# Performance work log

Measured on AMD Instinct MI355X. Metric: run time of the kernel, lower is better.

## Reference

```python
import jax, jax.numpy as jnp
import numpy as np

NUM_SAMPLES = 100  # hard-coded in the original forward


def _bilinear(img, x, y):
    """Bilinear sample img (H,W) at pixel coords x,y (any shape); border padding.
    Matches F.grid_sample(align_corners=True, padding_mode='border') since the
    original normalizes by (W-1)/(H-1) which maps back to the same pixel coords."""
    H, W = img.shape
    x0 = jnp.floor(x); y0 = jnp.floor(y)
    wx = x - x0; wy = y - y0
    x0i = jnp.clip(x0, 0, W - 1).astype(jnp.int32)
    x1i = jnp.clip(x0 + 1, 0, W - 1).astype(jnp.int32)
    y0i = jnp.clip(y0, 0, H - 1).astype(jnp.int32)
    y1i = jnp.clip(y0 + 1, 0, H - 1).astype(jnp.int32)
    return (img[y0i, x0i] * (1 - wx) * (1 - wy)
            + img[y0i, x1i] * wx * (1 - wy)
            + img[y1i, x0i] * (1 - wx) * wy
            + img[y1i, x1i] * wx * wy)


def setup_inputs() -> dict:
    key = jax.random.key(0)
    k1, k2, k3 = jax.random.split(key, 3)
    H = W = 2048
    N = 100000
    distance_image = jax.random.uniform(k1, (H, W), dtype=jnp.float32)
    points = jax.random.uniform(k2, (N, 2), dtype=jnp.float32) * (H - 1)
    normals = jax.random.normal(k3, (N, 2), dtype=jnp.float32)
    return {"distance_image": distance_image, "points": points, "normals": normals}


def reference(distance_image, points, normals):
    H, W = distance_image.shape
    N = points.shape[0]
    # original clamps both coords to [0, max(H-1, W-1)]
    pts = jnp.clip(points, 0.0, float(max(H - 1, W - 1)))  # (N,2)

    # direction perpendicular to normal, normalized
    d = jnp.stack([-normals[:, 1], normals[:, 0]], axis=-1)
    d = d / jnp.linalg.norm(d, axis=-1, keepdims=True)  # (N,2)
    dx, dy = d[:, 0], d[:, 1]
    px, py = pts[:, 0], pts[:, 1]

    maxf = jnp.finfo(d.dtype).max
    sdx = jnp.where(dx != 0, dx, 1.0)
    sdy = jnp.where(dy != 0, dy, 1.0)
    t_left = jnp.where(dx != 0, (0.0 - px) / sdx, -maxf)
    t_right = jnp.where(dx != 0, (W - 1.0 - px) / sdx, maxf)
    t_top = jnp.where(dy != 0, (0.0 - py) / sdy, -maxf)
    t_bottom = jnp.where(dy != 0, (H - 1.0 - py) / sdy, maxf)
    t_min = jnp.maximum(t_left, t_top)
    t_max = jnp.minimum(t_right, t_bottom)

    p1 = pts + t_min[:, None] * d  # (N,2)
    p2 = pts + t_max[:, None] * d  # (N,2)

    ts = jnp.linspace(0.0, 1.0, NUM_SAMPLES, dtype=pts.dtype)  # (S,)
    line = p1[:, None, :] + ts[None, :, None] * (p2 - p1)[:, None, :]  # (N,S,2)
    lx = jnp.clip(line[..., 0], 0.0, W - 1.0)
    ly = jnp.clip(line[..., 1], 0.0, H - 1.0)
    line = jnp.stack([lx, ly], axis=-1)  # clamped sampled points (N,S,2)

    vals = _bilinear(distance_image, lx, ly)  # (N,S)
    ref_val = _bilinear(distance_image, px, py)  # (N,)

    # local minima: strict minimum vs both neighbors, indices shifted by +1
    center = vals[:, 1:-1]
    minima = (center < vals[:, :-2]) & (center < vals[:, 2:])  # (N,S-2)

    # distance from each candidate (interior sample points) to the reference point
    dist = jnp.linalg.norm(line[:, 1:-1, :] - pts[:, None, :], axis=-1)  # (N,S-2)
    dist = jnp.where(minima, dist, jnp.inf)
    nearest = jnp.argmin(dist, axis=1)  # (N,)
    nearest_val = vals[jnp.arange(N), nearest + 1]  # (N,)

    # per-point mse of two scalars, then mean over points
    return jnp.mean((nearest_val - ref_val) ** 2)
```

## Files before the change

### kernel.cpp

```cpp
#include <hip/hip_runtime.h>
#include <float.h>
#include <math.h>

#define NSAMP 100
#define IMG_W 2048
#define IMG_H 2048

typedef _Float16 h2_t __attribute__((ext_vector_type(2), aligned(4)));
typedef _Float16 h4_t __attribute__((ext_vector_type(4), aligned(8)));
typedef _Float16 h8_t __attribute__((ext_vector_type(8), aligned(16)));

__global__ __launch_bounds__(256) void convert_kernel(const float* __restrict__ in,
                                                      h2_t* __restrict__ V,
                                                      double* __restrict__ accum,
                                                      unsigned int* __restrict__ done) {
    int idx = blockIdx.x * blockDim.x + threadIdx.x;
    if (idx == 0) { *accum = 0.0; *done = 0u; }
    int y  = idx >> 9;
    int x4 = (idx & 511) << 2;
    int y1 = min(y + 1, IMG_H - 1);
    float4 a = *(const float4*)(in + (size_t)y  * IMG_W + x4);
    float4 b = *(const float4*)(in + (size_t)y1 * IMG_W + x4);
    h8_t o;
    o[0] = (_Float16)a.x; o[1] = (_Float16)b.x;
    o[2] = (_Float16)a.y; o[3] = (_Float16)b.y;
    o[4] = (_Float16)a.z; o[5] = (_Float16)b.z;
    o[6] = (_Float16)a.w; o[7] = (_Float16)b.w;
    *(h8_t*)(V + (size_t)y * IMG_W + x4) = o;
}

__device__ __forceinline__ float bilinV(const h2_t* __restrict__ V, float x, float y) {
    float x0f = floorf(x), y0f = floorf(y);
    float wx = x - x0f, wy = y - y0f;
    int x0 = (int)x0f;
    int y0 = (int)y0f;
    int xa = min(x0, IMG_W - 2);
    bool edge = (x0 == IMG_W - 1);
    h4_t q = *(const h4_t*)(V + (size_t)y0 * IMG_W + xa);
    float v00 = edge ? (float)q[2] : (float)q[0];
    float v10 = edge ? (float)q[3] : (float)q[1];
    float v01 = (float)q[2];
    float v11 = (float)q[3];
    return v00 * (1.f - wx) * (1.f - wy) + v01 * wx * (1.f - wy)
         + v10 * (1.f - wx) * wy       + v11 * wx * wy;
}

__device__ __forceinline__ float tparam(int s) {
    return (s == NSAMP - 1) ? 1.0f : (float)((double)s * (1.0 / 99.0));
}

__global__ __launch_bounds__(256) void contour_loss_kernel(
        const h2_t* __restrict__ V,
        const float* __restrict__ points,
        const float* __restrict__ normals,
        double* __restrict__ accum,
        unsigned int* __restrict__ done,
        float* __restrict__ out,
        int N, int nblocks) {
    int i = blockIdx.x * blockDim.x + threadIdx.x;
    float sq = 0.f;
    if (i < N) {
        float px = fminf(fmaxf(points[2 * i],     0.f), 2047.f);
        float py = fminf(fmaxf(points[2 * i + 1], 0.f), 2047.f);
        float nx = normals[2 * i];
        float ny = normals[2 * i + 1];
        float ddx = -ny, ddy = nx;
        float nrm = sqrtf(ddx * ddx + ddy * ddy);
        float dx = ddx / nrm, dy = ddy / nrm;

        const float maxf = FLT_MAX;
        float sdx = (dx != 0.f) ? dx : 1.f;
        float sdy = (dy != 0.f) ? dy : 1.f;
        float t_left   = (dx != 0.f) ? (0.f    - px) / sdx : -maxf;
        float t_right  = (dx != 0.f) ? (2047.f - px) / sdx :  maxf;
        float t_top    = (dy != 0.f) ? (0.f    - py) / sdy : -maxf;
        float t_bottom = (dy != 0.f) ? (2047.f - py) / sdy :  maxf;
        float t_min = fmaxf(t_left, t_top);
        float t_max = fminf(t_right, t_bottom);

        float p1x = px + t_min * dx, p1y = py + t_min * dy;
        float p2x = px + t_max * dx, p2y = py + t_max * dy;
        float vx = p2x - p1x, vy = p2y - p1y;

        float ref_val = bilinV(V, px, py);

        float lx = fminf(fmaxf(p1x, 0.f), 2047.f);
        float ly = fminf(fmaxf(p1y, 0.f), 2047.f);
        float v_im1 = bilinV(V, lx, ly);
        float t1 = tparam(1);
        lx = fminf(fmaxf(p1x + t1 * vx, 0.f), 2047.f);
        ly = fminf(fmaxf(p1y + t1 * vy, 0.f), 2047.f);
        float v_i = bilinV(V, lx, ly);
        float cx = lx, cy = ly;

        float best_val = v_i;
        float best_d2  = INFINITY;

        #pragma unroll 8
        for (int s = 2; s < NSAMP; ++s) {
            float ts = tparam(s);
            float nlx = fminf(fmaxf(p1x + ts * vx, 0.f), 2047.f);
            float nly = fminf(fmaxf(p1y + ts * vy, 0.f), 2047.f);
            float v_ip1 = bilinV(V, nlx, nly);
            if (v_i < v_im1 && v_i < v_ip1) {
                float ex = cx - px, ey = cy - py;
                float d2 = ex * ex + ey * ey;
                if (d2 < best_d2) { best_d2 = d2; best_val = v_i; }
            }
            v_im1 = v_i; v_i = v_ip1; cx = nlx; cy = nly;
        }
        float diff = best_val - ref_val;
        sq = diff * diff;
    }

    for (int off = 32; off > 0; off >>= 1)
        sq += __shfl_down(sq, off);
    __shared__ float wsum[4];
    int lane = threadIdx.x & 63;
    int wid  = threadIdx.x >> 6;
    if (lane == 0) wsum[wid] = sq;
    __syncthreads();
    if (threadIdx.x == 0) {
        float bs = wsum[0] + wsum[1] + wsum[2] + wsum[3];
        atomicAdd(accum, (double)bs);
        __threadfence();
        unsigned int prev = atomicAdd(done, 1u);
        if (prev == (unsigned int)(nblocks - 1)) {
            double total = atomicAdd(accum, 0.0);
            out[0] = (float)(total / (double)N);
        }
    }
}

extern "C" void kernel_launch(void* const* d_in, const int* in_sizes, int n_in,
                              void* d_out, int out_size, void* d_ws, size_t ws_size,
                              hipStream_t stream) {
    const float* img     = (const float*)d_in[0];
    const float* points  = (const float*)d_in[1];
    const float* normals = (const float*)d_in[2];
    int N = in_sizes[1] / 2;
    float* out = (float*)d_out;

    char* ws = (char*)d_ws;
    h2_t* V = (h2_t*)ws;
    size_t off = (size_t)IMG_W * IMG_H * sizeof(h2_t);
    double* accum      = (double*)(ws + off);  off += 8;
    unsigned int* done = (unsigned int*)(ws + off);

    int conv_blocks = (IMG_W * IMG_H / 4) / 256;
    convert_kernel<<<conv_blocks, 256, 0, stream>>>(img, V, accum, done);

    int grid = (N + 255) / 256;
    contour_loss_kernel<<<grid, 256, 0, stream>>>(V, points, normals,
                                                  accum, done, out, N, grid);
}
```

Before: 128.9 us.

## Split each line's samples across four lanes with shuffle-based argmin merge

Each point is now handled by four consecutive threads, each scanning a 25-sample chunk of the line, followed by an xor-shuffle reduction that picks the nearest minimum and breaks ties by index. The goal is more parallelism: with only 100k points, the old one-thread-per-point launch gave few waves and a long serial latency chain of gathers. In exchange, each point's setup math and reference sample are recomputed four times, and each chunk boundary adds extra gathers.

```diff
diff --git a/kernel.cpp b/kernel.cpp
--- a/kernel.cpp
+++ b/kernel.cpp
@@ -5,6 +5,8 @@
 #define NSAMP 100
 #define IMG_W 2048
 #define IMG_H 2048
+#define LPP 4
+#define CPL 25
 
 typedef _Float16 h2_t __attribute__((ext_vector_type(2), aligned(4)));
 typedef _Float16 h4_t __attribute__((ext_vector_type(4), aligned(8)));
@@ -57,14 +59,16 @@
         unsigned int* __restrict__ done,
         float* __restrict__ out,
         int N, int nblocks) {
-    int i = blockIdx.x * blockDim.x + threadIdx.x;
+    int tid = blockIdx.x * blockDim.x + threadIdx.x;
+    int p = tid >> 2;
+    int k = tid & 3;
     float sq = 0.f;
-    if (i < N) {
-        float px = fminf(fmaxf(points[2 * i],     0.f), 2047.f);
-        float py = fminf(fmaxf(points[2 * i + 1], 0.f), 2047.f);
-        float nx = normals[2 * i];
-        float ny = normals[2 * i + 1];
-        float ddx = -ny, ddy = nx;
+    if (p < N) {
+        float2 pt = *(const float2*)(points  + 2 * (size_t)p);
+        float2 nm = *(const float2*)(normals + 2 * (size_t)p);
+        float px = fminf(fmaxf(pt.x, 0.f), 2047.f);
+        float py = fminf(fmaxf(pt.y, 0.f), 2047.f);
+        float ddx = -nm.y, ddy = nm.x;
         float nrm = sqrtf(ddx * ddx + ddy * ddy);
         float dx = ddx / nrm, dy = ddy / nrm;
 
@@ -84,33 +88,54 @@
 
         float ref_val = bilinV(V, px, py);
 
-        float lx = fminf(fmaxf(p1x, 0.f), 2047.f);
-        float ly = fminf(fmaxf(p1y, 0.f), 2047.f);
-        float v_im1 = bilinV(V, lx, ly);
-        float t1 = tparam(1);
-        lx = fminf(fmaxf(p1x + t1 * vx, 0.f), 2047.f);
-        ly = fminf(fmaxf(p1y + t1 * vy, 0.f), 2047.f);
-        float v_i = bilinV(V, lx, ly);
-        float cx = lx, cy = ly;
+        int cbase = k * CPL;
+        int sm1 = cbase - 1; if (sm1 < 0) sm1 = 0;
+        float ts = tparam(sm1);
+        float blx = fminf(fmaxf(p1x + ts * vx, 0.f), 2047.f);
+        float bly = fminf(fmaxf(p1y + ts * vy, 0.f), 2047.f);
+        float v_im1 = bilinV(V, blx, bly);
+        ts = tparam(cbase);
+        float cx = fminf(fmaxf(p1x + ts * vx, 0.f), 2047.f);
+        float cy = fminf(fmaxf(p1y + ts * vy, 0.f), 2047.f);
+        float v_i = bilinV(V, cx, cy);
 
-        float best_val = v_i;
+        float best_val = 0.f;
         float best_d2  = INFINITY;
+        int   best_idx = 0x7FFFFFFF;
+        float val_s1   = 0.f;
 
-        #pragma unroll 8
-        for (int s = 2; s < NSAMP; ++s) {
-            float ts = tparam(s);
-            float nlx = fminf(fmaxf(p1x + ts * vx, 0.f), 2047.f);
-            float nly = fminf(fmaxf(p1y + ts * vy, 0.f), 2047.f);
+        #pragma unroll 5
+        for (int j = 0; j < CPL; ++j) {
+            int c = cbase + j;
+            int sn = c + 1; if (sn > NSAMP - 1) sn = NSAMP - 1;
+            float tsn = tparam(sn);
+            float nlx = fminf(fmaxf(p1x + tsn * vx, 0.f), 2047.f);
+            float nly = fminf(fmaxf(p1y + tsn * vy, 0.f), 2047.f);
             float v_ip1 = bilinV(V, nlx, nly);
-            if (v_i < v_im1 && v_i < v_ip1) {
+            if (c == 1) val_s1 = v_i;
+            if (c >= 1 && c <= NSAMP - 2 && v_i < v_im1 && v_i < v_ip1) {
                 float ex = cx - px, ey = cy - py;
                 float d2 = ex * ex + ey * ey;
-                if (d2 < best_d2) { best_d2 = d2; best_val = v_i; }
+                if (d2 < best_d2) { best_d2 = d2; best_val = v_i; best_idx = c; }
             }
             v_im1 = v_i; v_i = v_ip1; cx = nlx; cy = nly;
         }
-        float diff = best_val - ref_val;
-        sq = diff * diff;
+
+        #pragma unroll
+        for (int m = 1; m < LPP; m <<= 1) {
+            float od2  = __shfl_xor(best_d2, m);
+            float oval = __shfl_xor(best_val, m);
+            int   oidx = __shfl_xor(best_idx, m);
+            if (od2 < best_d2 || (od2 == best_d2 && oidx < best_idx)) {
+                best_d2 = od2; best_val = oval; best_idx = oidx;
+            }
+        }
+
+        if (k == 0) {
+            if (best_idx == 0x7FFFFFFF) best_val = val_s1;
+            float diff = best_val - ref_val;
+            sq = diff * diff;
+        }
     }
 
     for (int off = 32; off > 0; off >>= 1)
@@ -150,7 +175,7 @@
     int conv_blocks = (IMG_W * IMG_H / 4) / 256;
     convert_kernel<<<conv_blocks, 256, 0, stream>>>(img, V, accum, done);
 
-    int grid = (N + 255) / 256;
+    int grid = (4 * N + 255) / 256;
     contour_loss_kernel<<<grid, 256, 0, stream>>>(V, points, normals,
                                                   accum, done, out, N, grid);
 }
```

New measurement: 180.4 us. 40.0% more time.

## Store image as plain fp16 and fetch two rows per bilinear sample

Applied to the files above, without the earlier changes.

Replaces the interleaved row-pair fp16 table (4 bytes per pixel) with a plain fp16 copy of the image (2 bytes per pixel). This halves the convert kernel's write traffic and the gather kernel's working set. In exchange, each bilinear sample now issues two 4-byte-aligned 8-byte loads, one per row, instead of one, with extra select logic for odd x. Point and normal loads are also vectorized to float2.

```diff
diff --git a/kernel.cpp b/kernel.cpp
--- a/kernel.cpp
+++ b/kernel.cpp
@@ -6,41 +6,39 @@
 #define IMG_W 2048
 #define IMG_H 2048
 
-typedef _Float16 h2_t __attribute__((ext_vector_type(2), aligned(4)));
-typedef _Float16 h4_t __attribute__((ext_vector_type(4), aligned(8)));
-typedef _Float16 h8_t __attribute__((ext_vector_type(8), aligned(16)));
+typedef _Float16 h4w_t __attribute__((ext_vector_type(4), aligned(8)));
+typedef _Float16 h4r_t __attribute__((ext_vector_type(4), aligned(4)));
 
 __global__ __launch_bounds__(256) void convert_kernel(const float* __restrict__ in,
-                                                      h2_t* __restrict__ V,
+                                                      _Float16* __restrict__ T,
                                                       double* __restrict__ accum,
                                                       unsigned int* __restrict__ done) {
     int idx = blockIdx.x * blockDim.x + threadIdx.x;
     if (idx == 0) { *accum = 0.0; *done = 0u; }
     int y  = idx >> 9;
     int x4 = (idx & 511) << 2;
-    int y1 = min(y + 1, IMG_H - 1);
-    float4 a = *(const float4*)(in + (size_t)y  * IMG_W + x4);
-    float4 b = *(const float4*)(in + (size_t)y1 * IMG_W + x4);
-    h8_t o;
-    o[0] = (_Float16)a.x; o[1] = (_Float16)b.x;
-    o[2] = (_Float16)a.y; o[3] = (_Float16)b.y;
-    o[4] = (_Float16)a.z; o[5] = (_Float16)b.z;
-    o[6] = (_Float16)a.w; o[7] = (_Float16)b.w;
-    *(h8_t*)(V + (size_t)y * IMG_W + x4) = o;
+    float4 a = *(const float4*)(in + (size_t)y * IMG_W + x4);
+    h4w_t o;
+    o[0] = (_Float16)a.x; o[1] = (_Float16)a.y;
+    o[2] = (_Float16)a.z; o[3] = (_Float16)a.w;
+    *(h4w_t*)(T + (size_t)y * IMG_W + x4) = o;
 }
 
-__device__ __forceinline__ float bilinV(const h2_t* __restrict__ V, float x, float y) {
+__device__ __forceinline__ float bilinT(const _Float16* __restrict__ T, float x, float y) {
     float x0f = floorf(x), y0f = floorf(y);
     float wx = x - x0f, wy = y - y0f;
     int x0 = (int)x0f;
     int y0 = (int)y0f;
-    int xa = min(x0, IMG_W - 2);
+    int y1 = min(y0 + 1, IMG_H - 1);
+    int xa = x0 & ~1;
+    bool odd  = (x0 & 1) != 0;
     bool edge = (x0 == IMG_W - 1);
-    h4_t q = *(const h4_t*)(V + (size_t)y0 * IMG_W + xa);
-    float v00 = edge ? (float)q[2] : (float)q[0];
-    float v10 = edge ? (float)q[3] : (float)q[1];
-    float v01 = (float)q[2];
-    float v11 = (float)q[3];
+    h4r_t r0 = *(const h4r_t*)(T + (y0 << 11) + xa);
+    h4r_t r1 = *(const h4r_t*)(T + (y1 << 11) + xa);
+    float v00 = odd ? (float)r0[1] : (float)r0[0];
+    float v10 = odd ? (float)r1[1] : (float)r1[0];
+    float v01 = edge ? (float)r0[1] : (odd ? (float)r0[2] : (float)r0[1]);
+    float v11 = edge ? (float)r1[1] : (odd ? (float)r1[2] : (float)r1[1]);
     return v00 * (1.f - wx) * (1.f - wy) + v01 * wx * (1.f - wy)
          + v10 * (1.f - wx) * wy       + v11 * wx * wy;
 }
@@ -50,7 +48,7 @@
 }
 
 __global__ __launch_bounds__(256) void contour_loss_kernel(
-        const h2_t* __restrict__ V,
+        const _Float16* __restrict__ T,
         const float* __restrict__ points,
         const float* __restrict__ normals,
         double* __restrict__ accum,
@@ -60,11 +58,11 @@
     int i = blockIdx.x * blockDim.x + threadIdx.x;
     float sq = 0.f;
     if (i < N) {
-        float px = fminf(fmaxf(points[2 * i],     0.f), 2047.f);
-        float py = fminf(fmaxf(points[2 * i + 1], 0.f), 2047.f);
-        float nx = normals[2 * i];
-        float ny = normals[2 * i + 1];
-        float ddx = -ny, ddy = nx;
+        float2 pt = *(const float2*)(points  + 2 * (size_t)i);
+        float2 nm = *(const float2*)(normals + 2 * (size_t)i);
+        float px = fminf(fmaxf(pt.x, 0.f), 2047.f);
+        float py = fminf(fmaxf(pt.y, 0.f), 2047.f);
+        float ddx = -nm.y, ddy = nm.x;
         float nrm = sqrtf(ddx * ddx + ddy * ddy);
         float dx = ddx / nrm, dy = ddy / nrm;
 
@@ -82,15 +80,15 @@
         float p2x = px + t_max * dx, p2y = py + t_max * dy;
         float vx = p2x - p1x, vy = p2y - p1y;
 
-        float ref_val = bilinV(V, px, py);
+        float ref_val = bilinT(T, px, py);
 
         float lx = fminf(fmaxf(p1x, 0.f), 2047.f);
         float ly = fminf(fmaxf(p1y, 0.f), 2047.f);
-        float v_im1 = bilinV(V, lx, ly);
+        float v_im1 = bilinT(T, lx, ly);
         float t1 = tparam(1);
         lx = fminf(fmaxf(p1x + t1 * vx, 0.f), 2047.f);
         ly = fminf(fmaxf(p1y + t1 * vy, 0.f), 2047.f);
-        float v_i = bilinV(V, lx, ly);
+        float v_i = bilinT(T, lx, ly);
         float cx = lx, cy = ly;
 
         float best_val = v_i;
@@ -101,7 +99,7 @@
             float ts = tparam(s);
             float nlx = fminf(fmaxf(p1x + ts * vx, 0.f), 2047.f);
             float nly = fminf(fmaxf(p1y + ts * vy, 0.f), 2047.f);
-            float v_ip1 = bilinV(V, nlx, nly);
+            float v_ip1 = bilinT(T, nlx, nly);
             if (v_i < v_im1 && v_i < v_ip1) {
                 float ex = cx - px, ey = cy - py;
                 float d2 = ex * ex + ey * ey;
@@ -142,15 +140,15 @@
     float* out = (float*)d_out;
 
     char* ws = (char*)d_ws;
-    h2_t* V = (h2_t*)ws;
-    size_t off = (size_t)IMG_W * IMG_H * sizeof(h2_t);
+    _Float16* T = (_Float16*)ws;
+    size_t off = (size_t)16 * 1024 * 1024;
     double* accum      = (double*)(ws + off);  off += 8;
     unsigned int* done = (unsigned int*)(ws + off);
 
     int conv_blocks = (IMG_W * IMG_H / 4) / 256;
-    convert_kernel<<<conv_blocks, 256, 0, stream>>>(img, V, accum, done);
+    convert_kernel<<<conv_blocks, 256, 0, stream>>>(img, T, accum, done);
 
     int grid = (N + 255) / 256;
-    contour_loss_kernel<<<grid, 256, 0, stream>>>(V, points, normals,
+    contour_loss_kernel<<<grid, 256, 0, stream>>>(T, points, normals,
                                                   accum, done, out, N, grid);
 }
```

Measured after the change: 155.6 us. 1.21x slower.

## Use 64-thread blocks with striped atomic accumulators and vectorized point loads

Applied to the files above, without the earlier changes.

Shrinks the loss kernel to one wavefront per block, which removes the shared-memory block reduction and barrier and spreads the work over more blocks. The per-block partial sums go to eight padded double accumulators instead of one, to reduce contention on a single atomic address, and the last block adds the slots together. It also loads points and normals as float2, uses a 32-bit shift for the row offset, and raises the unroll factor. The cost is four times as many blocks, and therefore four times as many atomics on the done counter.

```diff
diff --git a/kernel.cpp b/kernel.cpp
--- a/kernel.cpp
+++ b/kernel.cpp
@@ -5,6 +5,8 @@
 #define NSAMP 100
 #define IMG_W 2048
 #define IMG_H 2048
+#define NSLOT 8
+#define SLOT_STRIDE 16
 
 typedef _Float16 h2_t __attribute__((ext_vector_type(2), aligned(4)));
 typedef _Float16 h4_t __attribute__((ext_vector_type(4), aligned(8)));
@@ -15,7 +17,11 @@
                                                       double* __restrict__ accum,
                                                       unsigned int* __restrict__ done) {
     int idx = blockIdx.x * blockDim.x + threadIdx.x;
-    if (idx == 0) { *accum = 0.0; *done = 0u; }
+    if (idx == 0) {
+        #pragma unroll
+        for (int s = 0; s < NSLOT; ++s) accum[s * SLOT_STRIDE] = 0.0;
+        *done = 0u;
+    }
     int y  = idx >> 9;
     int x4 = (idx & 511) << 2;
     int y1 = min(y + 1, IMG_H - 1);
@@ -36,7 +42,7 @@
     int y0 = (int)y0f;
     int xa = min(x0, IMG_W - 2);
     bool edge = (x0 == IMG_W - 1);
-    h4_t q = *(const h4_t*)(V + (size_t)y0 * IMG_W + xa);
+    h4_t q = *(const h4_t*)(V + (y0 << 11) + xa);
     float v00 = edge ? (float)q[2] : (float)q[0];
     float v10 = edge ? (float)q[3] : (float)q[1];
     float v01 = (float)q[2];
@@ -49,7 +55,7 @@
     return (s == NSAMP - 1) ? 1.0f : (float)((double)s * (1.0 / 99.0));
 }
 
-__global__ __launch_bounds__(256) void contour_loss_kernel(
+__global__ __launch_bounds__(64) void contour_loss_kernel(
         const h2_t* __restrict__ V,
         const float* __restrict__ points,
         const float* __restrict__ normals,
@@ -60,11 +66,11 @@
     int i = blockIdx.x * blockDim.x + threadIdx.x;
     float sq = 0.f;
     if (i < N) {
-        float px = fminf(fmaxf(points[2 * i],     0.f), 2047.f);
-        float py = fminf(fmaxf(points[2 * i + 1], 0.f), 2047.f);
-        float nx = normals[2 * i];
-        float ny = normals[2 * i + 1];
-        float ddx = -ny, ddy = nx;
+        float2 pt = *(const float2*)(points  + 2 * (size_t)i);
+        float2 nm = *(const float2*)(normals + 2 * (size_t)i);
+        float px = fminf(fmaxf(pt.x, 0.f), 2047.f);
+        float py = fminf(fmaxf(pt.y, 0.f), 2047.f);
+        float ddx = -nm.y, ddy = nm.x;
         float nrm = sqrtf(ddx * ddx + ddy * ddy);
         float dx = ddx / nrm, dy = ddy / nrm;
 
@@ -96,7 +102,7 @@
         float best_val = v_i;
         float best_d2  = INFINITY;
 
-        #pragma unroll 8
+        #pragma unroll 14
         for (int s = 2; s < NSAMP; ++s) {
             float ts = tparam(s);
             float nlx = fminf(fmaxf(p1x + ts * vx, 0.f), 2047.f);
@@ -115,18 +121,15 @@
 
     for (int off = 32; off > 0; off >>= 1)
         sq += __shfl_down(sq, off);
-    __shared__ float wsum[4];
-    int lane = threadIdx.x & 63;
-    int wid  = threadIdx.x >> 6;
-    if (lane == 0) wsum[wid] = sq;
-    __syncthreads();
     if (threadIdx.x == 0) {
-        float bs = wsum[0] + wsum[1] + wsum[2] + wsum[3];
-        atomicAdd(accum, (double)bs);
+        atomicAdd(&accum[(blockIdx.x & (NSLOT - 1)) * SLOT_STRIDE], (double)sq);
         __threadfence();
         unsigned int prev = atomicAdd(done, 1u);
         if (prev == (unsigned int)(nblocks - 1)) {
-            double total = atomicAdd(accum, 0.0);
+            double total = 0.0;
+            #pragma unroll
+            for (int s = 0; s < NSLOT; ++s)
+                total += atomicAdd(&accum[s * SLOT_STRIDE], 0.0);
             out[0] = (float)(total / (double)N);
         }
     }
@@ -144,13 +147,13 @@
     char* ws = (char*)d_ws;
     h2_t* V = (h2_t*)ws;
     size_t off = (size_t)IMG_W * IMG_H * sizeof(h2_t);
-    double* accum      = (double*)(ws + off);  off += 8;
+    double* accum      = (double*)(ws + off);  off += NSLOT * SLOT_STRIDE * sizeof(double);
     unsigned int* done = (unsigned int*)(ws + off);
 
     int conv_blocks = (IMG_W * IMG_H / 4) / 256;
     convert_kernel<<<conv_blocks, 256, 0, stream>>>(img, V, accum, done);
 
-    int grid = (N + 255) / 256;
-    contour_loss_kernel<<<grid, 256, 0, stream>>>(V, points, normals,
-                                                  accum, done, out, N, grid);
+    int grid = (N + 63) / 64;
+    contour_loss_kernel<<<grid, 64, 0, stream>>>(V, points, normals,
+                                                 accum, done, out, N, grid);
 }
```

New measurement: 147.5 us. 1.14x slower.
